# Kernel tuning notes

Measured on AMD Instinct MI355X. Metric: run time of the kernel, lower is better.

The kernel has to match this reference:

```python
import jax, jax.numpy as jnp
import numpy as np

B, S, D = 32, 2048, 256


def _gru_cell(x, h, w_ih, w_hh, b_ih, b_hh):
    # PyTorch GRUCell math: gates ordered (reset, update, new)
    gi = x @ w_ih.T + b_ih          # [B, 3D]
    gh = h @ w_hh.T + b_hh          # [B, 3D]
    i_r, i_z, i_n = jnp.split(gi, 3, axis=-1)
    h_r, h_z, h_n = jnp.split(gh, 3, axis=-1)
    r = jax.nn.sigmoid(i_r + h_r)
    z = jax.nn.sigmoid(i_z + h_z)
    n = jnp.tanh(i_n + r * h_n)
    return (1.0 - z) * n + z * h


def setup_inputs() -> dict:
    key = jax.random.key(0)
    ks = jax.random.split(key, 5)
    scale = 1.0 / np.sqrt(D)
    return {
        "v_in": jax.random.normal(ks[0], (B, S, D), jnp.float32),
        "w_ih_f": jax.random.normal(ks[1], (3 * D, D), jnp.float32) * scale,
        "w_hh_f": jax.random.normal(ks[2], (3 * D, D), jnp.float32) * scale,
        "b_ih_f": jnp.zeros((3 * D,), jnp.float32),
        "b_hh_f": jnp.zeros((3 * D,), jnp.float32),
        "w_ih_b": jax.random.normal(ks[3], (3 * D, D), jnp.float32) * scale,
        "w_hh_b": jax.random.normal(ks[4], (3 * D, D), jnp.float32) * scale,
        "b_ih_b": jnp.zeros((3 * D,), jnp.float32),
        "b_hh_b": jnp.zeros((3 * D,), jnp.float32),
        "context_length": 10,
    }


def reference(v_in, w_ih_f, w_hh_f, b_ih_f, b_hh_f,
              w_ih_b, w_hh_b, b_ih_b, b_hh_b, context_length):
    d = w_ih_f.shape[1]
    v = v_in[:, :, :d]                      # v_tr in original
    vt = jnp.transpose(v, (1, 0, 2))        # [S, B, D], time-major for scan
    b, s = v.shape[0], v.shape[1]
    h0 = jnp.zeros((b, d), v.dtype)

    def step_f(h, x):
        h2 = _gru_cell(x, h, w_ih_f, w_hh_f, b_ih_f, b_hh_f)
        return h2, h2

    def step_b(h, x):
        h2 = _gru_cell(x, h, w_ih_b, w_hh_b, b_ih_b, b_hh_b)
        return h2, h2

    _, hf = jax.lax.scan(step_f, h0, vt)    # hf[t]: fwd state after step t
    vrev = vt[::-1]
    _, hb = jax.lax.scan(step_b, h0, vrev)  # hb[t]: bwd state at loop iter t

    cl = context_length
    sl = slice(cl, s - cl)
    # row i of h_enc is produced at loop t = i + cl:
    #   [h_f(t) + v[t], h_b(t) + v[S-1-t]]
    h_enc = jnp.concatenate([hf[sl] + vt[sl], hb[sl] + vrev[sl]], axis=-1)
    return jnp.transpose(h_enc, (1, 0, 2))  # [B, S-2*cl, 2D]
```

## Files before the change

### kernel.cpp

```cpp
#include <hip/hip_runtime.h>
#include <hip/hip_bf16.h>

typedef __attribute__((ext_vector_type(8))) short bf8_t;
typedef __attribute__((ext_vector_type(4))) float f32x4;

#define S_LEN 2048
#define BATCH 32
#define DH    256
#define NROW3 768
#define NCOL  1536

static __device__ __forceinline__ unsigned short f2bf(float f) {
  union { float f; unsigned u; } v; v.f = f;
  unsigned r = v.u + 0x7FFFu + ((v.u >> 16) & 1u);
  return (unsigned short)(r >> 16);
}
static __device__ __forceinline__ float bf2f(unsigned short u) {
  union { unsigned u; float f; } v; v.u = ((unsigned)u) << 16;
  return v.f;
}
static __device__ __forceinline__ float fast_sig(float x) {
  x = fminf(fmaxf(x, -30.f), 30.f);
  return __builtin_amdgcn_rcpf(1.f + __expf(-x));
}
static __device__ __forceinline__ float fast_tanh(float x) {
  x = fminf(fmaxf(x, -15.f), 15.f);
  float e = __expf(2.f * x);
  return (e - 1.f) * __builtin_amdgcn_rcpf(e + 1.f);
}
static __device__ __forceinline__ f32x4 MFMA(bf8_t a, bf8_t b, f32x4 c) {
  return __builtin_amdgcn_mfma_f32_16x16x32_bf16(a, b, c, 0, 0, 0);
}

__global__ __launch_bounds__(256) void gi_gemm(
    const float* __restrict__ X,
    const float* __restrict__ Wf, const float* __restrict__ Wb,
    const float* __restrict__ Bf, const float* __restrict__ Bb,
    unsigned short* __restrict__ gi)
{
  const int bid = blockIdx.x;
  const int nb = bid % 12, mb = bid / 12;
  const int m0 = mb * 128, n0 = nb * 128;
  const int tid = threadIdx.x;
  const int lane = tid & 63, wave = tid >> 6;
  const int wm = wave >> 1, wn = wave & 1;
  const int l15 = lane & 15, l4 = lane >> 4;

  __shared__ __align__(16) unsigned short As[128][40];
  __shared__ __align__(16) unsigned short Bs[128][40];

  f32x4 acc[4][4];
#pragma unroll
  for (int a = 0; a < 4; ++a)
#pragma unroll
    for (int c = 0; c < 4; ++c) acc[a][c] = f32x4{0.f, 0.f, 0.f, 0.f};

  float bias[4];
#pragma unroll
  for (int nt = 0; nt < 4; ++nt) {
    int c = n0 + wn * 64 + nt * 16 + l15;
    bias[nt] = (c < NROW3) ? Bf[c] : Bb[c - NROW3];
  }

  for (int k0 = 0; k0 < 256; k0 += 32) {
#pragma unroll
    for (int i = 0; i < 4; ++i) {
      int idx = tid + 256 * i;
      int r = idx >> 3, q = idx & 7;
      const float* pa = X + (size_t)(m0 + r) * 256 + k0 + q * 4;
      float4 va = *(const float4*)pa;
      unsigned long long pka =
          (unsigned long long)((unsigned)f2bf(va.x) | ((unsigned)f2bf(va.y) << 16)) |
          ((unsigned long long)((unsigned)f2bf(va.z) | ((unsigned)f2bf(va.w) << 16)) << 32);
      *(unsigned long long*)&As[r][q * 4] = pka;
      int cg = n0 + r;
      const float* pb = (cg < NROW3) ? (Wf + (size_t)cg * 256)
                                     : (Wb + (size_t)(cg - NROW3) * 256);
      float4 vb = *(const float4*)(pb + k0 + q * 4);
      unsigned long long pkb =
          (unsigned long long)((unsigned)f2bf(vb.x) | ((unsigned)f2bf(vb.y) << 16)) |
          ((unsigned long long)((unsigned)f2bf(vb.z) | ((unsigned)f2bf(vb.w) << 16)) << 32);
      *(unsigned long long*)&Bs[r][q * 4] = pkb;
    }
    __syncthreads();
    bf8_t af[4], bv[4];
#pragma unroll
    for (int mt = 0; mt < 4; ++mt)
      af[mt] = *(const bf8_t*)&As[wm * 64 + mt * 16 + l15][l4 * 8];
#pragma unroll
    for (int nt = 0; nt < 4; ++nt)
      bv[nt] = *(const bf8_t*)&Bs[wn * 64 + nt * 16 + l15][l4 * 8];
#pragma unroll
    for (int mt = 0; mt < 4; ++mt)
#pragma unroll
      for (int nt = 0; nt < 4; ++nt)
        acc[mt][nt] = MFMA(af[mt], bv[nt], acc[mt][nt]);
    __syncthreads();
  }
#pragma unroll
  for (int mt = 0; mt < 4; ++mt) {
#pragma unroll
    for (int nt = 0; nt < 4; ++nt) {
      int row = m0 + wm * 64 + mt * 16 + l4 * 4;
      int col = n0 + wn * 64 + nt * 16 + l15;
#pragma unroll
      for (int q = 0; q < 4; ++q)
        gi[(size_t)(row + q) * NCOL + col] = f2bf(acc[mt][nt][q] + bias[nt]);
    }
  }
}

__global__ __launch_bounds__(512) void rnn_rec(
    const float* __restrict__ v_in,
    const float* __restrict__ Whf, const float* __restrict__ Whb,
    const float* __restrict__ bhf, const float* __restrict__ bhb,
    const unsigned short* __restrict__ gi,
    const int* __restrict__ clp,
    float* __restrict__ out)
{
  const int bid = blockIdx.x;
  const int dir = bid & 1;
  const int b   = bid >> 1;
  const int tid = threadIdx.x;
  const int lane = tid & 63, wave = tid >> 6;
  const int l15 = lane & 15, l4 = lane >> 4;
  const int cl = clp[0];
  const int rows_out = S_LEN - 2 * cl;

  const float* W   = dir ? Whb : Whf;
  const float* bhh = dir ? bhb : bhf;

  __shared__ __align__(16) unsigned short h_lds[DH];
  __shared__ float gh_lds[NROW3];

  bf8_t afrag[6][8];
#pragma unroll
  for (int m = 0; m < 6; ++m) {
    const int row = (wave * 6 + m) * 16 + l15;
    const float* wr = W + (size_t)row * 256 + l4 * 8;
#pragma unroll
    for (int c = 0; c < 8; ++c) {
      const float* src = wr + c * 32;
      bf8_t f;
#pragma unroll
      for (int j = 0; j < 8; ++j) f[j] = (short)f2bf(src[j]);
      afrag[m][c] = f;
    }
  }

  if (tid < DH) h_lds[tid] = 0;
  float h_reg = 0.f;
  float bh_r = 0.f, bh_z = 0.f, bh_n = 0.f;
  const size_t vbase = (size_t)b * S_LEN * DH;
  const unsigned short* gib = gi + (size_t)b * S_LEN * NCOL + dir * NROW3;

  unsigned short p_r = 0, p_z = 0, p_n = 0;
  float p_v = 0.f;
  if (tid < DH) {
    bh_r = bhh[tid]; bh_z = bhh[DH + tid]; bh_n = bhh[2 * DH + tid];
    const int t0 = dir ? (S_LEN - 1) : 0;
    const unsigned short* g = gib + (size_t)t0 * NCOL;
    p_r = g[tid]; p_z = g[DH + tid]; p_n = g[2 * DH + tid];
    p_v = v_in[vbase + (size_t)t0 * DH + tid];
  }
  __syncthreads();

#pragma unroll 1
  for (int s = 0; s < S_LEN; ++s) {
    const float gir = bf2f(p_r), giz = bf2f(p_z), gin = bf2f(p_n), vv = p_v;
    if (tid < DH && s + 1 < S_LEN) {
      const int tn = dir ? (S_LEN - 2 - s) : (s + 1);
      const unsigned short* g = gib + (size_t)tn * NCOL;
      p_r = g[tid]; p_z = g[DH + tid]; p_n = g[2 * DH + tid];
      p_v = v_in[vbase + (size_t)tn * DH + tid];
    }

    f32x4 acc[6];
#pragma unroll
    for (int m = 0; m < 6; ++m) acc[m] = f32x4{0.f, 0.f, 0.f, 0.f};
#pragma unroll
    for (int c = 0; c < 8; ++c) {
      bf8_t bv = *(const bf8_t*)&h_lds[c * 32 + l4 * 8];
#pragma unroll
      for (int m = 0; m < 6; ++m) acc[m] = MFMA(afrag[m][c], bv, acc[m]);
    }
    if (l15 == 0) {
#pragma unroll
      for (int m = 0; m < 6; ++m) {
        const int rb = (wave * 6 + m) * 16 + l4 * 4;
        gh_lds[rb + 0] = acc[m][0];
        gh_lds[rb + 1] = acc[m][1];
        gh_lds[rb + 2] = acc[m][2];
        gh_lds[rb + 3] = acc[m][3];
      }
    }
    __syncthreads();
    if (tid < DH) {
      const float r = fast_sig(gh_lds[tid] + bh_r + gir);
      const float z = fast_sig(gh_lds[DH + tid] + bh_z + giz);
      const float n = fast_tanh(gin + r * (gh_lds[2 * DH + tid] + bh_n));
      const float h2 = (1.f - z) * n + z * h_reg;
      h_reg = h2;
      h_lds[tid] = f2bf(h2);
      if (s >= cl && s < S_LEN - cl) {
        out[((size_t)b * rows_out + (s - cl)) * (2 * DH) + dir * DH + tid] = h2 + vv;
      }
    }
    __syncthreads();
  }
}

extern "C" void kernel_launch(void* const* d_in, const int* in_sizes, int n_in,
                              void* d_out, int out_size, void* d_ws, size_t ws_size,
                              hipStream_t stream) {
  const float* v_in   = (const float*)d_in[0];
  const float* w_ih_f = (const float*)d_in[1];
  const float* w_hh_f = (const float*)d_in[2];
  const float* b_ih_f = (const float*)d_in[3];
  const float* b_hh_f = (const float*)d_in[4];
  const float* w_ih_b = (const float*)d_in[5];
  const float* w_hh_b = (const float*)d_in[6];
  const float* b_ih_b = (const float*)d_in[7];
  const float* b_hh_b = (const float*)d_in[8];
  const int*   clp    = (const int*)d_in[9];
  float* out = (float*)d_out;
  unsigned short* gi = (unsigned short*)d_ws;

  gi_gemm<<<dim3(512 * 12), dim3(256), 0, stream>>>(
      v_in, w_ih_f, w_ih_b, b_ih_f, b_ih_b, gi);
  rnn_rec<<<dim3(64), dim3(512), 0, stream>>>(
      v_in, w_hh_f, w_hh_b, b_hh_f, b_hh_b, gi, clp, out);
}
```

Baseline: 3.271 ms.

## Fuse input GEMM and GRU recurrence into one kernel with chunk flags

Replaces the two-kernel design with a single persistent kernel. Four blocks run the recurrence while the rest compute the input-projection GEMM in time chunks ordered from both ends and signal completion through atomic flags, so the recurrence can start before the whole GEMM finishes. The recurrence is also restructured: each block now handles 16 batch elements as the MFMA N dimension instead of one, which cuts the number of serial blocks. The r/z hidden biases are folded into the GEMM output, and stores are vectorized. The cost is spin-waiting on flags and a dependence on the recurrence blocks being scheduled first. Only four blocks drive the serial loop, each doing more work per step.

```diff
diff --git a/kernel.cpp b/kernel.cpp
--- a/kernel.cpp
+++ b/kernel.cpp
@@ -1,14 +1,13 @@
 #include <hip/hip_runtime.h>
-#include <hip/hip_bf16.h>
 
 typedef __attribute__((ext_vector_type(8))) short bf8_t;
 typedef __attribute__((ext_vector_type(4))) float f32x4;
+typedef __attribute__((ext_vector_type(4))) unsigned short us4;
 
 #define S_LEN 2048
-#define BATCH 32
-#define DH    256
-#define NROW3 768
-#define NCOL  1536
+#define NCHUNK 16
+#define CHUNK_TARGET 384u
+#define GI_BYTES (65536ULL * 1536ULL * 2ULL)
 
 static __device__ __forceinline__ unsigned short f2bf(float f) {
   union { float f; unsigned u; } v; v.f = f;
@@ -19,192 +18,217 @@
   union { unsigned u; float f; } v; v.u = ((unsigned)u) << 16;
   return v.f;
 }
-static __device__ __forceinline__ float fast_sig(float x) {
-  x = fminf(fmaxf(x, -30.f), 30.f);
+static __device__ __forceinline__ float sigm(float x) {
+  x = fminf(fmaxf(x, -20.f), 20.f);
   return __builtin_amdgcn_rcpf(1.f + __expf(-x));
 }
-static __device__ __forceinline__ float fast_tanh(float x) {
-  x = fminf(fmaxf(x, -15.f), 15.f);
+static __device__ __forceinline__ float tanh_(float x) {
+  x = fminf(fmaxf(x, -20.f), 20.f);
   float e = __expf(2.f * x);
-  return (e - 1.f) * __builtin_amdgcn_rcpf(e + 1.f);
+  return 1.f - 2.f * __builtin_amdgcn_rcpf(e + 1.f);
 }
 static __device__ __forceinline__ f32x4 MFMA(bf8_t a, bf8_t b, f32x4 c) {
   return __builtin_amdgcn_mfma_f32_16x16x32_bf16(a, b, c, 0, 0, 0);
 }
 
-__global__ __launch_bounds__(256) void gi_gemm(
-    const float* __restrict__ X,
-    const float* __restrict__ Wf, const float* __restrict__ Wb,
-    const float* __restrict__ Bf, const float* __restrict__ Bb,
-    unsigned short* __restrict__ gi)
-{
-  const int bid = blockIdx.x;
-  const int nb = bid % 12, mb = bid / 12;
-  const int m0 = mb * 128, n0 = nb * 128;
-  const int tid = threadIdx.x;
-  const int lane = tid & 63, wave = tid >> 6;
-  const int wm = wave >> 1, wn = wave & 1;
-  const int l15 = lane & 15, l4 = lane >> 4;
-
-  __shared__ __align__(16) unsigned short As[128][40];
-  __shared__ __align__(16) unsigned short Bs[128][40];
-
-  f32x4 acc[4][4];
-#pragma unroll
-  for (int a = 0; a < 4; ++a)
-#pragma unroll
-    for (int c = 0; c < 4; ++c) acc[a][c] = f32x4{0.f, 0.f, 0.f, 0.f};
-
-  float bias[4];
-#pragma unroll
-  for (int nt = 0; nt < 4; ++nt) {
-    int c = n0 + wn * 64 + nt * 16 + l15;
-    bias[nt] = (c < NROW3) ? Bf[c] : Bb[c - NROW3];
-  }
-
-  for (int k0 = 0; k0 < 256; k0 += 32) {
-#pragma unroll
-    for (int i = 0; i < 4; ++i) {
-      int idx = tid + 256 * i;
-      int r = idx >> 3, q = idx & 7;
-      const float* pa = X + (size_t)(m0 + r) * 256 + k0 + q * 4;
-      float4 va = *(const float4*)pa;
-      unsigned long long pka =
-          (unsigned long long)((unsigned)f2bf(va.x) | ((unsigned)f2bf(va.y) << 16)) |
-          ((unsigned long long)((unsigned)f2bf(va.z) | ((unsigned)f2bf(va.w) << 16)) << 32);
-      *(unsigned long long*)&As[r][q * 4] = pka;
-      int cg = n0 + r;
-      const float* pb = (cg < NROW3) ? (Wf + (size_t)cg * 256)
-                                     : (Wb + (size_t)(cg - NROW3) * 256);
-      float4 vb = *(const float4*)(pb + k0 + q * 4);
-      unsigned long long pkb =
-          (unsigned long long)((unsigned)f2bf(vb.x) | ((unsigned)f2bf(vb.y) << 16)) |
-          ((unsigned long long)((unsigned)f2bf(vb.z) | ((unsigned)f2bf(vb.w) << 16)) << 32);
-      *(unsigned long long*)&Bs[r][q * 4] = pkb;
-    }
-    __syncthreads();
-    bf8_t af[4], bv[4];
-#pragma unroll
-    for (int mt = 0; mt < 4; ++mt)
-      af[mt] = *(const bf8_t*)&As[wm * 64 + mt * 16 + l15][l4 * 8];
-#pragma unroll
-    for (int nt = 0; nt < 4; ++nt)
-      bv[nt] = *(const bf8_t*)&Bs[wn * 64 + nt * 16 + l15][l4 * 8];
-#pragma unroll
-    for (int mt = 0; mt < 4; ++mt)
-#pragma unroll
-      for (int nt = 0; nt < 4; ++nt)
-        acc[mt][nt] = MFMA(af[mt], bv[nt], acc[mt][nt]);
-    __syncthreads();
-  }
-#pragma unroll
-  for (int mt = 0; mt < 4; ++mt) {
-#pragma unroll
-    for (int nt = 0; nt < 4; ++nt) {
-      int row = m0 + wm * 64 + mt * 16 + l4 * 4;
-      int col = n0 + wn * 64 + nt * 16 + l15;
-#pragma unroll
-      for (int q = 0; q < 4; ++q)
-        gi[(size_t)(row + q) * NCOL + col] = f2bf(acc[mt][nt][q] + bias[nt]);
-    }
-  }
-}
-
-__global__ __launch_bounds__(512) void rnn_rec(
+__global__ void zero_flags_k(unsigned int* f) {
+  if (threadIdx.x < NCHUNK) f[threadIdx.x] = 0u;
+}
+
+__global__ __launch_bounds__(512, 2) void fused_k(
     const float* __restrict__ v_in,
-    const float* __restrict__ Whf, const float* __restrict__ Whb,
-    const float* __restrict__ bhf, const float* __restrict__ bhb,
-    const unsigned short* __restrict__ gi,
+    const float* __restrict__ Wif, const float* __restrict__ Whf,
+    const float* __restrict__ bif, const float* __restrict__ bhf,
+    const float* __restrict__ Wib, const float* __restrict__ Whb,
+    const float* __restrict__ bib, const float* __restrict__ bhb,
     const int* __restrict__ clp,
+    unsigned short* __restrict__ gi,
+    unsigned int* flags,
     float* __restrict__ out)
 {
   const int bid = blockIdx.x;
-  const int dir = bid & 1;
-  const int b   = bid >> 1;
   const int tid = threadIdx.x;
   const int lane = tid & 63, wave = tid >> 6;
   const int l15 = lane & 15, l4 = lane >> 4;
+
+  __shared__ __align__(16) unsigned short As[128][40];
+  __shared__ __align__(16) unsigned short Bs[128][40];
+  __shared__ __align__(16) unsigned short hlds[16][264];
+
+  if (bid >= 4) {
+    const int gidb = bid - 4;
+    const int cr = gidb / 384, sub = gidb % 384;
+    const int bb = sub / 12, nb = sub % 12;
+    const int c = (cr & 1) ? (15 - (cr >> 1)) : (cr >> 1);
+    const int m0 = bb * 2048 + c * 128;
+    const int n0 = nb * 128;
+    const int wm = wave >> 2, wn = wave & 3;
+
+    f32x4 acc[4][2];
+#pragma unroll
+    for (int a = 0; a < 4; ++a)
+#pragma unroll
+      for (int b = 0; b < 2; ++b) acc[a][b] = f32x4{0.f, 0.f, 0.f, 0.f};
+
+    for (int k0 = 0; k0 < 256; k0 += 32) {
+#pragma unroll
+      for (int i = 0; i < 2; ++i) {
+        int u = tid + 512 * i;
+        int r = u >> 3, q = u & 7;
+        float4 va = *(const float4*)(v_in + (size_t)(m0 + r) * 256 + k0 + q * 4);
+        unsigned long long pka =
+            (unsigned long long)((unsigned)f2bf(va.x) | ((unsigned)f2bf(va.y) << 16)) |
+            ((unsigned long long)((unsigned)f2bf(va.z) | ((unsigned)f2bf(va.w) << 16)) << 32);
+        *(unsigned long long*)&As[r][q * 4] = pka;
+        int cg = n0 + r;
+        const float* pb = (cg < 768) ? (Wif + (size_t)cg * 256)
+                                     : (Wib + (size_t)(cg - 768) * 256);
+        float4 vbv = *(const float4*)(pb + k0 + q * 4);
+        unsigned long long pkb =
+            (unsigned long long)((unsigned)f2bf(vbv.x) | ((unsigned)f2bf(vbv.y) << 16)) |
+            ((unsigned long long)((unsigned)f2bf(vbv.z) | ((unsigned)f2bf(vbv.w) << 16)) << 32);
+        *(unsigned long long*)&Bs[r][q * 4] = pkb;
+      }
+      __syncthreads();
+      bf8_t af[4], bv2[2];
+#pragma unroll
+      for (int mt = 0; mt < 4; ++mt)
+        af[mt] = *(const bf8_t*)&As[wm * 64 + mt * 16 + l15][l4 * 8];
+#pragma unroll
+      for (int nt = 0; nt < 2; ++nt)
+        bv2[nt] = *(const bf8_t*)&Bs[wn * 32 + nt * 16 + l15][l4 * 8];
+#pragma unroll
+      for (int mt = 0; mt < 4; ++mt)
+#pragma unroll
+        for (int nt = 0; nt < 2; ++nt)
+          acc[mt][nt] = MFMA(af[mt], bv2[nt], acc[mt][nt]);
+      __syncthreads();
+    }
+#pragma unroll
+    for (int nt = 0; nt < 2; ++nt) {
+      int col = n0 + wn * 32 + nt * 16 + l15;
+      int col3 = (col < 768) ? col : col - 768;
+      int gate = col3 >> 8;
+      float bias = ((col < 768) ? bif[col3] : bib[col3]) +
+                   ((gate < 2) ? ((col < 768) ? bhf[col3] : bhb[col3]) : 0.f);
+#pragma unroll
+      for (int mt = 0; mt < 4; ++mt) {
+        int row = m0 + wm * 64 + mt * 16 + l4 * 4;
+#pragma unroll
+        for (int q = 0; q < 4; ++q)
+          gi[(size_t)(row + q) * 1536 + col] = f2bf(acc[mt][nt][q] + bias);
+      }
+    }
+    __syncthreads();
+    if (tid == 0)
+      __hip_atomic_fetch_add(&flags[c], 1u, __ATOMIC_RELEASE, __HIP_MEMORY_SCOPE_AGENT);
+    return;
+  }
+
+  const int dir = bid & 1;
+  const int batch = (bid >> 1) * 16 + l15;
   const int cl = clp[0];
-  const int rows_out = S_LEN - 2 * cl;
-
-  const float* W   = dir ? Whb : Whf;
-  const float* bhh = dir ? bhb : bhf;
-
-  __shared__ __align__(16) unsigned short h_lds[DH];
-  __shared__ float gh_lds[NROW3];
-
-  bf8_t afrag[6][8];
-#pragma unroll
-  for (int m = 0; m < 6; ++m) {
-    const int row = (wave * 6 + m) * 16 + l15;
-    const float* wr = W + (size_t)row * 256 + l4 * 8;
+  const int rows = S_LEN - 2 * cl;
+  const float* Wh = dir ? Whb : Whf;
+  const float* bh = dir ? bhb : bhf;
+  const int h00 = wave * 16 + l4 * 4;
+  const int h01 = h00 + 128;
+
+  bf8_t A[8][6];
+#pragma unroll
+  for (int gg = 0; gg < 6; ++gg) {
+    const int g = gg >> 1, hg = gg & 1;
+    const int row = g * 256 + (wave + 8 * hg) * 16 + l15;
+    const float* wr = Wh + (size_t)row * 256 + l4 * 8;
 #pragma unroll
     for (int c = 0; c < 8; ++c) {
-      const float* src = wr + c * 32;
+      float4 w0 = *(const float4*)(wr + c * 32);
+      float4 w1 = *(const float4*)(wr + c * 32 + 4);
       bf8_t f;
-#pragma unroll
-      for (int j = 0; j < 8; ++j) f[j] = (short)f2bf(src[j]);
-      afrag[m][c] = f;
+      f[0] = (short)f2bf(w0.x); f[1] = (short)f2bf(w0.y);
+      f[2] = (short)f2bf(w0.z); f[3] = (short)f2bf(w0.w);
+      f[4] = (short)f2bf(w1.x); f[5] = (short)f2bf(w1.y);
+      f[6] = (short)f2bf(w1.z); f[7] = (short)f2bf(w1.w);
+      A[c][gg] = f;
     }
   }
-
-  if (tid < DH) h_lds[tid] = 0;
-  float h_reg = 0.f;
-  float bh_r = 0.f, bh_z = 0.f, bh_n = 0.f;
-  const size_t vbase = (size_t)b * S_LEN * DH;
-  const unsigned short* gib = gi + (size_t)b * S_LEN * NCOL + dir * NROW3;
-
-  unsigned short p_r = 0, p_z = 0, p_n = 0;
-  float p_v = 0.f;
-  if (tid < DH) {
-    bh_r = bhh[tid]; bh_z = bhh[DH + tid]; bh_n = bhh[2 * DH + tid];
-    const int t0 = dir ? (S_LEN - 1) : 0;
-    const unsigned short* g = gib + (size_t)t0 * NCOL;
-    p_r = g[tid]; p_z = g[DH + tid]; p_n = g[2 * DH + tid];
-    p_v = v_in[vbase + (size_t)t0 * DH + tid];
-  }
+  const f32x4 bhn0 = *(const f32x4*)(bh + 512 + h00);
+  const f32x4 bhn1 = *(const f32x4*)(bh + 512 + h01);
+
+  for (int i = tid; i < 16 * 264; i += 512) ((unsigned short*)hlds)[i] = 0;
   __syncthreads();
+
+  const unsigned short* gib = gi + (size_t)batch * S_LEN * 1536 + dir * 768;
+  const float* vb = v_in + (size_t)batch * S_LEN * 256;
+  float* ob = out + (size_t)batch * rows * 512 + dir * 256;
 
 #pragma unroll 1
   for (int s = 0; s < S_LEN; ++s) {
-    const float gir = bf2f(p_r), giz = bf2f(p_z), gin = bf2f(p_n), vv = p_v;
-    if (tid < DH && s + 1 < S_LEN) {
-      const int tn = dir ? (S_LEN - 2 - s) : (s + 1);
-      const unsigned short* g = gib + (size_t)tn * NCOL;
-      p_r = g[tid]; p_z = g[DH + tid]; p_n = g[2 * DH + tid];
-      p_v = v_in[vbase + (size_t)tn * DH + tid];
-    }
-
-    f32x4 acc[6];
-#pragma unroll
-    for (int m = 0; m < 6; ++m) acc[m] = f32x4{0.f, 0.f, 0.f, 0.f};
+    const int t = dir ? (S_LEN - 1 - s) : s;
+    if ((t & 127) == (dir ? 127 : 0)) {
+      if (tid == 0) {
+        unsigned int* fp = &flags[t >> 7];
+        while (__hip_atomic_load(fp, __ATOMIC_RELAXED, __HIP_MEMORY_SCOPE_AGENT) < CHUNK_TARGET)
+          __builtin_amdgcn_s_sleep(16);
+        (void)__hip_atomic_load(fp, __ATOMIC_ACQUIRE, __HIP_MEMORY_SCOPE_AGENT);
+      }
+      __syncthreads();
+    }
+    const unsigned short* gt = gib + (size_t)t * 1536;
+    const us4 LR0 = *(const us4*)(gt + h00);
+    const us4 LZ0 = *(const us4*)(gt + 256 + h00);
+    const us4 LN0 = *(const us4*)(gt + 512 + h00);
+    const us4 LR1 = *(const us4*)(gt + h01);
+    const us4 LZ1 = *(const us4*)(gt + 256 + h01);
+    const us4 LN1 = *(const us4*)(gt + 512 + h01);
+    const float* vt = vb + (size_t)t * 256;
+    const float4 V0 = *(const float4*)(vt + h00);
+    const float4 V1 = *(const float4*)(vt + h01);
+    const us4 HO0 = *(const us4*)&hlds[l15][h00];
+    const us4 HO1 = *(const us4*)&hlds[l15][h01];
+
+    f32x4 aR0 = {0.f,0.f,0.f,0.f}, aZ0 = aR0, aN0 = aR0;
+    f32x4 aR1 = aR0, aZ1 = aR0, aN1 = aR0;
 #pragma unroll
     for (int c = 0; c < 8; ++c) {
-      bf8_t bv = *(const bf8_t*)&h_lds[c * 32 + l4 * 8];
-#pragma unroll
-      for (int m = 0; m < 6; ++m) acc[m] = MFMA(afrag[m][c], bv, acc[m]);
-    }
-    if (l15 == 0) {
-#pragma unroll
-      for (int m = 0; m < 6; ++m) {
-        const int rb = (wave * 6 + m) * 16 + l4 * 4;
-        gh_lds[rb + 0] = acc[m][0];
-        gh_lds[rb + 1] = acc[m][1];
-        gh_lds[rb + 2] = acc[m][2];
-        gh_lds[rb + 3] = acc[m][3];
-      }
+      const bf8_t bv = *(const bf8_t*)&hlds[l15][c * 32 + l4 * 8];
+      aR0 = MFMA(A[c][0], bv, aR0);
+      aR1 = MFMA(A[c][1], bv, aR1);
+      aZ0 = MFMA(A[c][2], bv, aZ0);
+      aZ1 = MFMA(A[c][3], bv, aZ1);
+      aN0 = MFMA(A[c][4], bv, aN0);
+      aN1 = MFMA(A[c][5], bv, aN1);
     }
     __syncthreads();
-    if (tid < DH) {
-      const float r = fast_sig(gh_lds[tid] + bh_r + gir);
-      const float z = fast_sig(gh_lds[DH + tid] + bh_z + giz);
-      const float n = fast_tanh(gin + r * (gh_lds[2 * DH + tid] + bh_n));
-      const float h2 = (1.f - z) * n + z * h_reg;
-      h_reg = h2;
-      h_lds[tid] = f2bf(h2);
-      if (s >= cl && s < S_LEN - cl) {
-        out[((size_t)b * rows_out + (s - cl)) * (2 * DH) + dir * DH + tid] = h2 + vv;
-      }
+
+    float h20[4], h21[4];
+#pragma unroll
+    for (int q = 0; q < 4; ++q) {
+      const float r = sigm(aR0[q] + bf2f(LR0[q]));
+      const float z = sigm(aZ0[q] + bf2f(LZ0[q]));
+      const float n = tanh_(bf2f(LN0[q]) + r * (aN0[q] + bhn0[q]));
+      const float ho = bf2f(HO0[q]);
+      h20[q] = n + z * (ho - n);
+    }
+#pragma unroll
+    for (int q = 0; q < 4; ++q) {
+      const float r = sigm(aR1[q] + bf2f(LR1[q]));
+      const float z = sigm(aZ1[q] + bf2f(LZ1[q]));
+      const float n = tanh_(bf2f(LN1[q]) + r * (aN1[q] + bhn1[q]));
+      const float ho = bf2f(HO1[q]);
+      h21[q] = n + z * (ho - n);
+    }
+    us4 w0, w1;
+    w0[0] = f2bf(h20[0]); w0[1] = f2bf(h20[1]); w0[2] = f2bf(h20[2]); w0[3] = f2bf(h20[3]);
+    w1[0] = f2bf(h21[0]); w1[1] = f2bf(h21[1]); w1[2] = f2bf(h21[2]); w1[3] = f2bf(h21[3]);
+    *(us4*)&hlds[l15][h00] = w0;
+    *(us4*)&hlds[l15][h01] = w1;
+
+    if (s >= cl && s < S_LEN - cl) {
+      const float4 o0 = {h20[0] + V0.x, h20[1] + V0.y, h20[2] + V0.z, h20[3] + V0.w};
+      const float4 o1 = {h21[0] + V1.x, h21[1] + V1.y, h21[2] + V1.z, h21[3] + V1.w};
+      *(float4*)(ob + (size_t)(s - cl) * 512 + h00) = o0;
+      *(float4*)(ob + (size_t)(s - cl) * 512 + h01) = o1;
     }
     __syncthreads();
   }
@@ -225,9 +249,10 @@
   const int*   clp    = (const int*)d_in[9];
   float* out = (float*)d_out;
   unsigned short* gi = (unsigned short*)d_ws;
-
-  gi_gemm<<<dim3(512 * 12), dim3(256), 0, stream>>>(
-      v_in, w_ih_f, w_ih_b, b_ih_f, b_ih_b, gi);
-  rnn_rec<<<dim3(64), dim3(512), 0, stream>>>(
-      v_in, w_hh_f, w_hh_b, b_hh_f, b_hh_b, gi, clp, out);
-}
+  unsigned int* flags = (unsigned int*)((char*)d_ws + GI_BYTES);
+
+  zero_flags_k<<<dim3(1), dim3(64), 0, stream>>>(flags);
+  fused_k<<<dim3(4 + NCHUNK * 384), dim3(512), 0, stream>>>(
+      v_in, w_ih_f, w_hh_f, b_ih_f, b_hh_f,
+      w_ih_b, w_hh_b, b_ih_b, b_hh_b, clp, gi, flags, out);
+}
```

Measured after the change: 7.208 ms. 120% more time.
